# Kernel tuning notes

Hardware: AMD Instinct MI355X
Metric: run time of the kernel (lower is better)

Reference implementation:

```python
import jax, jax.numpy as jnp
import numpy as np

B, N, D, R, NUM_HEADS, S = 8, 512, 256, 6, 3, 1000


def setup_inputs() -> dict:
    key = jax.random.key(0)
    ks = jax.random.split(key, 12)
    init = lambda k, shape: jax.random.normal(k, shape, jnp.float32) * 0.02
    return {
        "symbol_ids": jax.random.randint(ks[0], (B, N), 0, S),
        "positions": jax.random.normal(ks[1], (B, N, 2), jnp.float32),
        "sym_table": init(ks[2], (S, D)),
        "layer_table": init(ks[3], (S, D)),      # layer-0 interpretation embedding
        "rel_W": init(ks[4], (R, D, D)),          # per-relation Linear weights (in,out)
        "rel_b": init(ks[5], (R, D)),
        "h1_W": init(ks[6], (NUM_HEADS, D, D)),   # interpretation head Linear1
        "h1_b": init(ks[7], (NUM_HEADS, D)),
        "h2_W": init(ks[8], (NUM_HEADS, D)),      # interpretation head Linear2 (D->1)
        "h2_b": init(ks[9], (NUM_HEADS,)),
        "out_W": init(ks[10], (D, D)),
        "out_b": init(ks[11], (D,)),
    }


def _relation_type(dx, dy):
    # Vectorized version of PositionalGrammar._get_relation_type (if/elif chain)
    return jnp.select(
        [dy > 0.5, dy < -0.5, dx < -0.5, dx > 0.5,
         (jnp.abs(dx) < 0.3) & (jnp.abs(dy) < 0.3)],
        [0, 1, 2, 3, 4], 5)


def _positional_grammar(symbols, positions, rel_W, rel_b):
    # transformed[b,j] = symbols[b,j] + sum_{i!=j} (symbols[b,i] @ W_r(i,j) + b_r(i,j))
    dx = positions[:, None, :, 0] - positions[:, :, None, 0]  # [b,i,j]
    dy = positions[:, None, :, 1] - positions[:, :, None, 1]
    rel = _relation_type(dx, dy)                               # [b,i,j] int
    n = symbols.shape[1]
    not_self = ~jnp.eye(n, dtype=bool)
    # one-hot relation mask, self-pairs excluded: [b,i,j,r]
    M = ((rel[..., None] == jnp.arange(R)) & not_self[None, :, :, None]).astype(symbols.dtype)
    T = jnp.einsum('bid,rde->brie', symbols, rel_W)            # per-relation transform of sources
    contrib = jnp.einsum('bijr,brie->bje', M, T)               # scatter-add over sources i
    bias = jnp.einsum('bijr,re->bje', M, rel_b)                # per-pair bias accumulation
    return symbols + contrib + bias


def reference(symbol_ids, positions, sym_table, layer_table, rel_W, rel_b,
              h1_W, h1_b, h2_W, h2_b, out_W, out_b):
    # SymbolEmbedding (calendar_pos=None path; layer=0)
    symbols = sym_table[symbol_ids] + layer_table[symbol_ids]  # [B,N,D]
    # PositionalGrammar
    symbols = _positional_grammar(symbols, positions, rel_W, rel_b)
    # LayeredInterpretation: 3 heads of Linear-GELU-Linear(D->1)
    h = jax.nn.gelu(jnp.einsum('bnd,rde->brne', symbols, h1_W)
                    + h1_b[None, :, None, :], approximate=False)
    interp = jnp.einsum('brne,re->brn', h, h2_W) + h2_b[None, :, None]  # [B,3,N]
    # output projection
    output = symbols @ out_W + out_b
    return (output,
            interp[:, 0, :, None],   # exoteric  [B,N,1]
            interp[:, 1, :, None],   # esoteric
            interp[:, 2, :, None],   # sacred
            symbols)
```

## Files before the change

kernel.cpp:

```cpp
#include <hip/hip_runtime.h>
#include <hip/hip_bf16.h>
#include <math.h>

#define BB 8
#define NN 512
#define DD 256
#define BNT 4096

typedef __attribute__((ext_vector_type(8))) short short8;
typedef __attribute__((ext_vector_type(4))) float f32x4;

#define OFF_S0B   0u
#define OFF_TT    524288u
#define OFF_WCT   6815744u
#define OFF_WBT   7012352u
#define OFF_BB    7143424u
#define OFF_REL   7144448u

#define OUT0_OFF   0u
#define INTERP_OFF 1048576u
#define SYM_OFF    1060864u

__device__ __forceinline__ float gelu_exact(float x) {
    return 0.5f * x * (1.0f + erff(x * 0.70710678118654752f));
}

__device__ __forceinline__ ushort f2bf(float x) {
    __hip_bfloat16 h = __float2bfloat16(x);
    union { __hip_bfloat16 b; ushort u; } cv;
    cv.b = h;
    return cv.u;
}

typedef __attribute__((address_space(3))) unsigned int  lds_u32;
typedef __attribute__((address_space(1))) unsigned int  glb_u32;
__device__ __forceinline__ void gload16(const void* g, void* l) {
    __builtin_amdgcn_global_load_lds((const glb_u32*)g, (lds_u32*)l, 16, 0, 0);
}

__device__ __forceinline__ int rel_of(float dx, float dy) {
    int r = (fabsf(dx) < 0.3f && fabsf(dy) < 0.3f) ? 4 : 5;
    r = (dx >  0.5f) ? 3 : r;
    r = (dx < -0.5f) ? 2 : r;
    r = (dy < -0.5f) ? 1 : r;
    r = (dy >  0.5f) ? 0 : r;
    return r;
}

__device__ __forceinline__ short8 onehot8(uint2 cw, unsigned rr) {
    union { ushort u[8]; short8 v; } o;
    unsigned m = rr * 0x01010101u;
    unsigned x = cw.x ^ m, y = cw.y ^ m;
#pragma unroll
    for (int t = 0; t < 4; t++) {
        o.u[t]     = (((x >> (8 * t)) & 255u) == 0u) ? 0x3F80 : 0;
        o.u[t + 4] = (((y >> (8 * t)) & 255u) == 0u) ? 0x3F80 : 0;
    }
    return o.v;
}

#define WAVE_IDS()                                             \
    const int lane = tid & 63, w = tid >> 6;                   \
    const int wm = w >> 1, wn = w & 1;                         \
    const int quad = lane >> 4, l15 = lane & 15;               \
    const int sm = tid >> 2, sq = tid & 3;                     \
    (void)sm; (void)sq;

#define ACC_INIT()                                             \
    f32x4 acc[2][2];                                           \
    _Pragma("unroll") for (int mt = 0; mt < 2; mt++)           \
    _Pragma("unroll") for (int nt = 0; nt < 2; nt++)           \
        acc[mt][nt] = (f32x4){0.f, 0.f, 0.f, 0.f};

#define MFMA4(a0, a1, b0, b1)                                                     \
    acc[0][0] = __builtin_amdgcn_mfma_f32_16x16x32_bf16(a0, b0, acc[0][0], 0, 0, 0); \
    acc[0][1] = __builtin_amdgcn_mfma_f32_16x16x32_bf16(a0, b1, acc[0][1], 0, 0, 0); \
    acc[1][0] = __builtin_amdgcn_mfma_f32_16x16x32_bf16(a1, b0, acc[1][0], 0, 0, 0); \
    acc[1][1] = __builtin_amdgcn_mfma_f32_16x16x32_bf16(a1, b1, acc[1][1], 0, 0, 0);

#define MFMA_STEP(Abuf, Bbuf)                                                \
    {                                                                        \
        short8 af[2], bfr[2];                                                \
        _Pragma("unroll")                                                    \
        for (int mt = 0; mt < 2; mt++)                                       \
            af[mt] = *(const short8*)&(Abuf)[(quad * 64 + wm * 32 + mt * 16 + l15) * 8]; \
        _Pragma("unroll")                                                    \
        for (int nt = 0; nt < 2; nt++)                                       \
            bfr[nt] = *(const short8*)&(Bbuf)[(quad * 64 + wn * 32 + nt * 16 + l15) * 8]; \
        MFMA4(af[0], af[1], bfr[0], bfr[1]);                                 \
    }

__global__ __launch_bounds__(256) void front_kernel(
    const int* __restrict__ ids, const float* __restrict__ positions,
    const float* __restrict__ symt, const float* __restrict__ layt,
    const float* __restrict__ relW, const float* __restrict__ h1W,
    const float* __restrict__ outW, const float* __restrict__ h1b,
    const float* __restrict__ outb, const float* __restrict__ h2b,
    ushort* __restrict__ WcT, ushort* __restrict__ WbT,
    float* __restrict__ bbig, float* __restrict__ outI,
    float* __restrict__ symOut, ushort* __restrict__ s0b,
    unsigned char* __restrict__ rel)
{
    __shared__ float px[NN], py[NN];
    int blk = blockIdx.x, tid = threadIdx.x;
    if (blk < 1536) {
        int idx = blk * 256 + tid;
        {
            int e = idx / 1536, k = idx - e * 1536;
            int r = k >> 8, d = k & 255;
            WcT[idx] = f2bf(relW[(r * DD + d) * DD + e]);
        }
        if (idx < 262144) {
            int c = idx >> 8, d = idx & 255;
            float v;
            if (c < 768) { int r = c >> 8, e = c & 255; v = h1W[(r * DD + d) * DD + e]; }
            else         { v = outW[d * DD + (c - 768)]; }
            WbT[idx] = f2bf(v);
        }
        if (idx < 3 * BNT) outI[idx] = h2b[idx >> 12];
        if (idx < 1024) bbig[idx] = (idx < 768) ? h1b[idx] : outb[idx - 768];
    } else if (blk < 2560) {
        int row = (blk - 1536) * 4 + (tid >> 6);
        int d = (tid & 63) * 4;
        int id = ids[row];
        float4 a = *(const float4*)&symt[(size_t)id * DD + d];
        float4 c = *(const float4*)&layt[(size_t)id * DD + d];
        float4 v = {a.x + c.x, a.y + c.y, a.z + c.z, a.w + c.w};
        *(float4*)&symOut[(size_t)row * DD + d] = v;
        union { ushort u[4]; uint2 q; } p;
        p.u[0] = f2bf(v.x); p.u[1] = f2bf(v.y); p.u[2] = f2bf(v.z); p.u[3] = f2bf(v.w);
        *(uint2*)&s0b[(size_t)row * DD + d] = p.q;
    } else {
        int blk2 = blk - 2560;
        int b = blk2 >> 6;
        int j0 = (blk2 & 63) << 3;
        int jl = tid >> 5, sub = tid & 31;
        for (int i = tid; i < NN; i += 256) {
            float2 p = ((const float2*)positions)[b * NN + i];
            px[i] = p.x; py[i] = p.y;
        }
        __syncthreads();
        int j = j0 + jl;
        float xj = px[j], yj = py[j];
        union { unsigned char u8[16]; uint4 v; } codes;
#pragma unroll
        for (int t = 0; t < 16; t++) {
            int i = sub * 16 + t;
            int r = rel_of(xj - px[i], yj - py[i]);
            r = (i == j) ? 6 : r;
            codes.u8[t] = (unsigned char)r;
        }
        *(uint4*)&rel[((size_t)(b * NN + j)) * NN + sub * 16] = codes.v;
    }
}

__global__ __launch_bounds__(256) void gemmT_kernel(
    const ushort* __restrict__ WcT, const ushort* __restrict__ s0b,
    const float* __restrict__ relb, ushort* __restrict__ TT)
{
    __shared__ ushort Als[2][2048], Bls[2][2048];
    int tid = threadIdx.x;
    int b = blockIdx.z;
    int rowM0 = blockIdx.y * 64;
    int col0 = blockIdx.x * 64;
    int r = rowM0 >> 8, e0 = rowM0 & 255;
    WAVE_IDS();
    ACC_INIT();
    const ushort* gA = WcT + (size_t)(e0 + lane) * 1536 + r * 256 + w * 8;
    const ushort* gB = s0b + ((size_t)(b * NN) + col0 + lane) * DD + w * 8;

    gload16(gA, &Als[0][w * 512]);
    gload16(gB, &Bls[0][w * 512]);
    __syncthreads();
#pragma unroll
    for (int s = 0; s < 8; s++) {
        if (s < 7) {
            gload16(gA + (s + 1) * 32, &Als[(s + 1) & 1][w * 512]);
            gload16(gB + (s + 1) * 32, &Bls[(s + 1) & 1][w * 512]);
        }
        MFMA_STEP(Als[s & 1], Bls[s & 1]);
        __syncthreads();
    }
#pragma unroll
    for (int mt = 0; mt < 2; mt++)
#pragma unroll
        for (int nt = 0; nt < 2; nt++)
#pragma unroll
            for (int v = 0; v < 4; v++) {
                int e = e0 + wm * 32 + mt * 16 + quad * 4 + v;
                int i = col0 + wn * 32 + nt * 16 + l15;
                TT[((size_t)(b * DD) + e) * 3072 + r * 512 + i] =
                    f2bf(acc[mt][nt][v] + relb[r * DD + e]);
            }
}

__global__ __launch_bounds__(256) void agg_gemm(
    const unsigned char* __restrict__ rel, const ushort* __restrict__ TT,
    float* __restrict__ symOut)
{
    __shared__ ushort Bls[2][2048];
    int tid = threadIdx.x;
    int z = blockIdx.z;
    int b = z / 6;
    unsigned rr = (unsigned)(z - b * 6);
    int row0 = blockIdx.y * 64, col0 = blockIdx.x * 64;
    WAVE_IDS();
    ACC_INIT();
    const ushort* gB = TT + ((size_t)(b * DD) + col0 + lane) * 3072 + rr * 512 + w * 8;
    const unsigned char* gC0 = rel + ((size_t)(b * NN) + row0 + wm * 32 + l15) * NN + quad * 8;
    const unsigned char* gC1 = gC0 + 16 * NN;

    gload16(gB, &Bls[0][w * 512]);
    uint2 c0 = *(const uint2*)gC0;
    uint2 c1 = *(const uint2*)gC1;
    __syncthreads();
#pragma unroll
    for (int s = 0; s < 16; s++) {
        uint2 n0 = c0, n1 = c1;
        if (s < 15) {
            gload16(gB + (s + 1) * 32, &Bls[(s + 1) & 1][w * 512]);
            n0 = *(const uint2*)(gC0 + (s + 1) * 32);
            n1 = *(const uint2*)(gC1 + (s + 1) * 32);
        }
        short8 a0 = onehot8(c0, rr);
        short8 a1 = onehot8(c1, rr);
        short8 b0 = *(const short8*)&Bls[s & 1][(quad * 64 + wn * 32 + l15) * 8];
        short8 b1 = *(const short8*)&Bls[s & 1][(quad * 64 + wn * 32 + 16 + l15) * 8];
        MFMA4(a0, a1, b0, b1);
        c0 = n0; c1 = n1;
        __syncthreads();
    }
#pragma unroll
    for (int mt = 0; mt < 2; mt++)
#pragma unroll
        for (int nt = 0; nt < 2; nt++)
#pragma unroll
            for (int v = 0; v < 4; v++) {
                int j = row0 + wm * 32 + mt * 16 + quad * 4 + v;
                int e = col0 + wn * 32 + nt * 16 + l15;
                atomicAdd(&symOut[((size_t)(b * NN) + j) * DD + e], acc[mt][nt][v]);
            }
}

__global__ __launch_bounds__(256) void gemm2_kernel(
    const float* __restrict__ symOut, const ushort* __restrict__ WbT,
    const float* __restrict__ bbig, const float* __restrict__ h2W,
    float* __restrict__ out0, float* __restrict__ outI)
{
    __shared__ ushort Als[2][2048], Bls[2][2048];
    int tid = threadIdx.x;
    int row0 = blockIdx.y * 64, col0 = blockIdx.x * 64;
    WAVE_IDS();
    ACC_INIT();
    const float*  gA = symOut + (size_t)(row0 + sm) * DD + sq * 8;
    const ushort* gB = WbT + (size_t)(col0 + lane) * DD + w * 8;
    const int lo = (sq * 64 + sm) * 8;

#define G2_STAGE(a0, a1, buf)                                       \
    {                                                               \
        union alignas(16) { ushort u[8]; uint4 v; } am;             \
        am.u[0] = f2bf(a0.x); am.u[1] = f2bf(a0.y);                 \
        am.u[2] = f2bf(a0.z); am.u[3] = f2bf(a0.w);                 \
        am.u[4] = f2bf(a1.x); am.u[5] = f2bf(a1.y);                 \
        am.u[6] = f2bf(a1.z); am.u[7] = f2bf(a1.w);                 \
        *(uint4*)&Als[buf][lo] = am.v;                              \
    }

    float4 a0 = *(const float4*)gA;
    float4 a1 = *(const float4*)(gA + 4);
    gload16(gB, &Bls[0][w * 512]);
    G2_STAGE(a0, a1, 0);
    __syncthreads();
#pragma unroll
    for (int s = 0; s < 8; s++) {
        float4 x = a0, y = a1;
        if (s < 7) {
            x = *(const float4*)(gA + (s + 1) * 32);
            y = *(const float4*)(gA + (s + 1) * 32 + 4);
            gload16(gB + (s + 1) * 32, &Bls[(s + 1) & 1][w * 512]);
        }
        MFMA_STEP(Als[s & 1], Bls[s & 1]);
        if (s < 7) { G2_STAGE(x, y, (s + 1) & 1); }
        __syncthreads();
    }
#undef G2_STAGE
    if (col0 >= 768) {
#pragma unroll
        for (int nt = 0; nt < 2; nt++) {
            int c = col0 + wn * 32 + nt * 16 + l15;
            float bb = bbig[c];
#pragma unroll
            for (int mt = 0; mt < 2; mt++)
#pragma unroll
                for (int v = 0; v < 4; v++) {
                    int row = row0 + wm * 32 + mt * 16 + quad * 4 + v;
                    out0[(size_t)row * DD + (c - 768)] = acc[mt][nt][v] + bb;
                }
        }
    } else {
        int head = col0 >> 8;
        float part[2][4];
#pragma unroll
        for (int mt = 0; mt < 2; mt++)
#pragma unroll
            for (int v = 0; v < 4; v++) part[mt][v] = 0.f;
#pragma unroll
        for (int nt = 0; nt < 2; nt++) {
            int c = col0 + wn * 32 + nt * 16 + l15;
            float bb = bbig[c];
            float w2 = h2W[c];
#pragma unroll
            for (int mt = 0; mt < 2; mt++)
#pragma unroll
                for (int v = 0; v < 4; v++)
                    part[mt][v] += gelu_exact(acc[mt][nt][v] + bb) * w2;
        }
#pragma unroll
        for (int mt = 0; mt < 2; mt++)
#pragma unroll
            for (int v = 0; v < 4; v++) {
                float p = part[mt][v];
                p += __shfl_xor(p, 1); p += __shfl_xor(p, 2);
                p += __shfl_xor(p, 4); p += __shfl_xor(p, 8);
                if (l15 == 0) {
                    int row = row0 + wm * 32 + mt * 16 + quad * 4 + v;
                    atomicAdd(&outI[head * BNT + row], p);
                }
            }
    }
}

extern "C" void kernel_launch(void* const* d_in, const int* in_sizes, int n_in,
                              void* d_out, int out_size, void* d_ws, size_t ws_size,
                              hipStream_t stream)
{
    const int*   ids  = (const int*)d_in[0];
    const float* pos  = (const float*)d_in[1];
    const float* symt = (const float*)d_in[2];
    const float* layt = (const float*)d_in[3];
    const float* relW = (const float*)d_in[4];
    const float* relb = (const float*)d_in[5];
    const float* h1W  = (const float*)d_in[6];
    const float* h1b  = (const float*)d_in[7];
    const float* h2W  = (const float*)d_in[8];
    const float* h2b  = (const float*)d_in[9];
    const float* outW = (const float*)d_in[10];
    const float* outb = (const float*)d_in[11];
    float* out = (float*)d_out;
    float* ws  = (float*)d_ws;

    ushort* s0b  = (ushort*)(ws + OFF_S0B);
    ushort* TT   = (ushort*)(ws + OFF_TT);
    ushort* WcT  = (ushort*)(ws + OFF_WCT);
    ushort* WbT  = (ushort*)(ws + OFF_WBT);
    float*  bbig = ws + OFF_BB;
    unsigned char* rel = (unsigned char*)(ws + OFF_REL);

    front_kernel<<<3072, 256, 0, stream>>>(ids, pos, symt, layt, relW, h1W, outW,
                                           h1b, outb, h2b, WcT, WbT, bbig,
                                           out + INTERP_OFF, out + SYM_OFF, s0b, rel);
    gemmT_kernel<<<dim3(8, 24, 8), 256, 0, stream>>>(WcT, s0b, relb, TT);
    agg_gemm<<<dim3(4, 8, 48), 256, 0, stream>>>(rel, TT, out + SYM_OFF);
    gemm2_kernel<<<dim3(16, 64), 256, 0, stream>>>(out + SYM_OFF, WbT,
                                                   bbig, h2W,
                                                   out + OUT0_OFF, out + INTERP_OFF);
}
```

Measured before the change: 157.7 us.

## Reorder relation aggregation before projection and compute bias from relation counts

The relation step now aggregates raw symbols per relation first (one-hot mask times transposed bf16 symbols) and then applies a single concatenated 4096x1536x256 projection against the stacked relation weights. This replaces the per-relation transform of all sources (the large TT buffer) followed by atomic scatter-adds. Per-target relation counts are computed with byte-match popcounts in the front kernel and turn the bias sum into six multiply-adds. The projection kernel does plain read-modify-write instead of atomics. The trade-off is an extra bf16 rounding of the aggregated Gc intermediate and a K=1536 GEMM with larger shared-memory tiles.

Result: slower. 163.0 us (+3.3%).

```diff
diff --git a/kernel.cpp b/kernel.cpp
--- a/kernel.cpp
+++ b/kernel.cpp
@@ -10,12 +10,13 @@
 typedef __attribute__((ext_vector_type(8))) short short8;
 typedef __attribute__((ext_vector_type(4))) float f32x4;
 
-#define OFF_S0B   0u
-#define OFF_TT    524288u
-#define OFF_WCT   6815744u
-#define OFF_WBT   7012352u
-#define OFF_BB    7143424u
-#define OFF_REL   7144448u
+#define OFF_S0T   0u
+#define OFF_GC    524288u
+#define OFF_WCT   3670016u
+#define OFF_WBT   3866624u
+#define OFF_BB    3997696u
+#define OFF_CNT   3998720u
+#define OFF_REL   4015104u
 
 #define OUT0_OFF   0u
 #define INTERP_OFF 1048576u
@@ -57,6 +58,10 @@
         o.u[t + 4] = (((y >> (8 * t)) & 255u) == 0u) ? 0x3F80 : 0;
     }
     return o.v;
+}
+
+__device__ __forceinline__ unsigned zbyte_mask(unsigned t) {
+    return ~(((t & 0x7F7F7F7Fu) + 0x7F7F7F7Fu) | t) & 0x80808080u;
 }
 
 #define WAVE_IDS()                                             \
@@ -98,10 +103,10 @@
     const float* __restrict__ outb, const float* __restrict__ h2b,
     ushort* __restrict__ WcT, ushort* __restrict__ WbT,
     float* __restrict__ bbig, float* __restrict__ outI,
-    float* __restrict__ symOut, ushort* __restrict__ s0b,
-    unsigned char* __restrict__ rel)
+    float* __restrict__ symOut, ushort* __restrict__ s0T,
+    unsigned char* __restrict__ rel, ushort* __restrict__ cnts)
 {
-    __shared__ float px[NN], py[NN];
+    __shared__ float shbuf[32 * 257];
     int blk = blockIdx.x, tid = threadIdx.x;
     if (blk < 1536) {
         int idx = blk * 256 + tid;
@@ -119,19 +124,36 @@
         }
         if (idx < 3 * BNT) outI[idx] = h2b[idx >> 12];
         if (idx < 1024) bbig[idx] = (idx < 768) ? h1b[idx] : outb[idx - 768];
-    } else if (blk < 2560) {
-        int row = (blk - 1536) * 4 + (tid >> 6);
-        int d = (tid & 63) * 4;
+    } else if (blk < 1664) {
+        int row0 = (blk - 1536) * 32;
+        int b = row0 >> 9, i0 = row0 & 511;
+        int rl = tid >> 3, dq = (tid & 7) * 4;
+        int row = row0 + rl;
         int id = ids[row];
-        float4 a = *(const float4*)&symt[(size_t)id * DD + d];
-        float4 c = *(const float4*)&layt[(size_t)id * DD + d];
-        float4 v = {a.x + c.x, a.y + c.y, a.z + c.z, a.w + c.w};
-        *(float4*)&symOut[(size_t)row * DD + d] = v;
-        union { ushort u[4]; uint2 q; } p;
-        p.u[0] = f2bf(v.x); p.u[1] = f2bf(v.y); p.u[2] = f2bf(v.z); p.u[3] = f2bf(v.w);
-        *(uint2*)&s0b[(size_t)row * DD + d] = p.q;
+#pragma unroll
+        for (int u = 0; u < 8; u++) {
+            int d = dq + u * 32;
+            float4 a = *(const float4*)&symt[(size_t)id * DD + d];
+            float4 c = *(const float4*)&layt[(size_t)id * DD + d];
+            float4 v = {a.x + c.x, a.y + c.y, a.z + c.z, a.w + c.w};
+            *(float4*)&symOut[(size_t)row * DD + d] = v;
+            shbuf[rl * 257 + d + 0] = v.x;
+            shbuf[rl * 257 + d + 1] = v.y;
+            shbuf[rl * 257 + d + 2] = v.z;
+            shbuf[rl * 257 + d + 3] = v.w;
+        }
+        __syncthreads();
+        int dd = tid;
+        union { ushort u[32]; uint4 q[4]; } pk;
+#pragma unroll
+        for (int ii = 0; ii < 32; ii++) pk.u[ii] = f2bf(shbuf[ii * 257 + dd]);
+        ushort* dst = s0T + ((size_t)(b * DD + dd)) * 512 + i0;
+#pragma unroll
+        for (int q = 0; q < 4; q++) ((uint4*)dst)[q] = pk.q[q];
     } else {
-        int blk2 = blk - 2560;
+        float* px = shbuf;
+        float* py = shbuf + NN;
+        int blk2 = blk - 1664;
         int b = blk2 >> 6;
         int j0 = (blk2 & 63) << 3;
         int jl = tid >> 5, sub = tid & 31;
@@ -142,7 +164,7 @@
         __syncthreads();
         int j = j0 + jl;
         float xj = px[j], yj = py[j];
-        union { unsigned char u8[16]; uint4 v; } codes;
+        union { unsigned char u8[16]; unsigned wd[4]; uint4 v; } codes;
 #pragma unroll
         for (int t = 0; t < 16; t++) {
             int i = sub * 16 + t;
@@ -151,85 +173,87 @@
             codes.u8[t] = (unsigned char)r;
         }
         *(uint4*)&rel[((size_t)(b * NN + j)) * NN + sub * 16] = codes.v;
-    }
-}
-
-__global__ __launch_bounds__(256) void gemmT_kernel(
-    const ushort* __restrict__ WcT, const ushort* __restrict__ s0b,
-    const float* __restrict__ relb, ushort* __restrict__ TT)
+        int cnt[6];
+#pragma unroll
+        for (int r = 0; r < 6; r++) {
+            unsigned m = (unsigned)r * 0x01010101u;
+            int c = 0;
+#pragma unroll
+            for (int k = 0; k < 4; k++)
+                c += __builtin_popcount(zbyte_mask(codes.wd[k] ^ m));
+            cnt[r] = c;
+        }
+#pragma unroll
+        for (int r = 0; r < 6; r++) {
+            cnt[r] += __shfl_xor(cnt[r], 1);
+            cnt[r] += __shfl_xor(cnt[r], 2);
+            cnt[r] += __shfl_xor(cnt[r], 4);
+            cnt[r] += __shfl_xor(cnt[r], 8);
+            cnt[r] += __shfl_xor(cnt[r], 16);
+        }
+        if (sub == 0) {
+            uint4 pq;
+            pq.x = (unsigned)cnt[0] | ((unsigned)cnt[1] << 16);
+            pq.y = (unsigned)cnt[2] | ((unsigned)cnt[3] << 16);
+            pq.z = (unsigned)cnt[4] | ((unsigned)cnt[5] << 16);
+            pq.w = 0u;
+            *(uint4*)&cnts[((size_t)(b * NN + j)) * 8] = pq;
+        }
+    }
+}
+
+__global__ __launch_bounds__(256) void aggT_kernel(
+    const unsigned char* __restrict__ rel, const ushort* __restrict__ s0T,
+    ushort* __restrict__ Gc)
 {
-    __shared__ ushort Als[2][2048], Bls[2][2048];
-    int tid = threadIdx.x;
-    int b = blockIdx.z;
-    int rowM0 = blockIdx.y * 64;
-    int col0 = blockIdx.x * 64;
-    int r = rowM0 >> 8, e0 = rowM0 & 255;
-    WAVE_IDS();
-    ACC_INIT();
-    const ushort* gA = WcT + (size_t)(e0 + lane) * 1536 + r * 256 + w * 8;
-    const ushort* gB = s0b + ((size_t)(b * NN) + col0 + lane) * DD + w * 8;
-
-    gload16(gA, &Als[0][w * 512]);
-    gload16(gB, &Bls[0][w * 512]);
-    __syncthreads();
-#pragma unroll
-    for (int s = 0; s < 8; s++) {
-        if (s < 7) {
-            gload16(gA + (s + 1) * 32, &Als[(s + 1) & 1][w * 512]);
-            gload16(gB + (s + 1) * 32, &Bls[(s + 1) & 1][w * 512]);
-        }
-        MFMA_STEP(Als[s & 1], Bls[s & 1]);
-        __syncthreads();
-    }
-#pragma unroll
-    for (int mt = 0; mt < 2; mt++)
-#pragma unroll
-        for (int nt = 0; nt < 2; nt++)
-#pragma unroll
-            for (int v = 0; v < 4; v++) {
-                int e = e0 + wm * 32 + mt * 16 + quad * 4 + v;
-                int i = col0 + wn * 32 + nt * 16 + l15;
-                TT[((size_t)(b * DD) + e) * 3072 + r * 512 + i] =
-                    f2bf(acc[mt][nt][v] + relb[r * DD + e]);
-            }
-}
-
-__global__ __launch_bounds__(256) void agg_gemm(
-    const unsigned char* __restrict__ rel, const ushort* __restrict__ TT,
-    float* __restrict__ symOut)
-{
-    __shared__ ushort Bls[2][2048];
+    __shared__ ushort Bls[2][4096];
     int tid = threadIdx.x;
     int z = blockIdx.z;
     int b = z / 6;
     unsigned rr = (unsigned)(z - b * 6);
-    int row0 = blockIdx.y * 64, col0 = blockIdx.x * 64;
+    int row0 = blockIdx.y * 64;
+    int col0 = blockIdx.x * 64;
     WAVE_IDS();
     ACC_INIT();
-    const ushort* gB = TT + ((size_t)(b * DD) + col0 + lane) * 3072 + rr * 512 + w * 8;
+    const ushort* gB = s0T + ((size_t)(b * DD) + col0 + lane) * 512 + w * 8;
     const unsigned char* gC0 = rel + ((size_t)(b * NN) + row0 + wm * 32 + l15) * NN + quad * 8;
     const unsigned char* gC1 = gC0 + 16 * NN;
 
-    gload16(gB, &Bls[0][w * 512]);
-    uint2 c0 = *(const uint2*)gC0;
-    uint2 c1 = *(const uint2*)gC1;
+#define AGT_STAGE(s, buf)                                     \
+    gload16(gB + (s) * 64,      &Bls[buf][ w      * 512]);    \
+    gload16(gB + (s) * 64 + 32, &Bls[buf][(w + 4) * 512]);
+
+    uint2 cc[2][2], cn[2][2];
+    cc[0][0] = *(const uint2*)(gC0);
+    cc[0][1] = *(const uint2*)(gC0 + 32);
+    cc[1][0] = *(const uint2*)(gC1);
+    cc[1][1] = *(const uint2*)(gC1 + 32);
+    AGT_STAGE(0, 0);
     __syncthreads();
 #pragma unroll
-    for (int s = 0; s < 16; s++) {
-        uint2 n0 = c0, n1 = c1;
-        if (s < 15) {
-            gload16(gB + (s + 1) * 32, &Bls[(s + 1) & 1][w * 512]);
-            n0 = *(const uint2*)(gC0 + (s + 1) * 32);
-            n1 = *(const uint2*)(gC1 + (s + 1) * 32);
-        }
-        short8 a0 = onehot8(c0, rr);
-        short8 a1 = onehot8(c1, rr);
-        short8 b0 = *(const short8*)&Bls[s & 1][(quad * 64 + wn * 32 + l15) * 8];
-        short8 b1 = *(const short8*)&Bls[s & 1][(quad * 64 + wn * 32 + 16 + l15) * 8];
-        MFMA4(a0, a1, b0, b1);
-        c0 = n0; c1 = n1;
+    for (int s = 0; s < 8; s++) {
+        if (s < 7) {
+            AGT_STAGE(s + 1, (s + 1) & 1);
+            cn[0][0] = *(const uint2*)(gC0 + (s + 1) * 64);
+            cn[0][1] = *(const uint2*)(gC0 + (s + 1) * 64 + 32);
+            cn[1][0] = *(const uint2*)(gC1 + (s + 1) * 64);
+            cn[1][1] = *(const uint2*)(gC1 + (s + 1) * 64 + 32);
+        }
+#pragma unroll
+        for (int h = 0; h < 2; h++) {
+            short8 a0 = onehot8(cc[0][h], rr);
+            short8 a1 = onehot8(cc[1][h], rr);
+            short8 b0 = *(const short8*)&Bls[s & 1][((h * 4 + quad) * 64 + wn * 32 + l15) * 8];
+            short8 b1 = *(const short8*)&Bls[s & 1][((h * 4 + quad) * 64 + wn * 32 + 16 + l15) * 8];
+            MFMA4(a0, a1, b0, b1);
+        }
+        if (s < 7) {
+            cc[0][0] = cn[0][0]; cc[0][1] = cn[0][1];
+            cc[1][0] = cn[1][0]; cc[1][1] = cn[1][1];
+        }
         __syncthreads();
     }
+#undef AGT_STAGE
 #pragma unroll
     for (int mt = 0; mt < 2; mt++)
 #pragma unroll
@@ -237,9 +261,67 @@
 #pragma unroll
             for (int v = 0; v < 4; v++) {
                 int j = row0 + wm * 32 + mt * 16 + quad * 4 + v;
+                int d = col0 + wn * 32 + nt * 16 + l15;
+                Gc[((size_t)(b * NN) + j) * 1536 + rr * 256 + d] =
+                    f2bf(acc[mt][nt][v]);
+            }
+}
+
+__global__ __launch_bounds__(256) void projC_kernel(
+    const ushort* __restrict__ Gc, const ushort* __restrict__ WcT,
+    const ushort* __restrict__ cnts, const float* __restrict__ relb,
+    float* __restrict__ symOut)
+{
+    __shared__ ushort Als[2][8192], Bls[2][8192];
+    int tid = threadIdx.x;
+    int row0 = blockIdx.y * 64;
+    int col0 = blockIdx.x * 64;
+    WAVE_IDS();
+    ACC_INIT();
+    const ushort* gA = Gc  + (size_t)(row0 + lane) * 1536 + w * 8;
+    const ushort* gB = WcT + (size_t)(col0 + lane) * 1536 + w * 8;
+
+#define PJ_STAGE(s, buf)                                                    \
+    _Pragma("unroll")                                                       \
+    for (int p = 0; p < 4; p++) {                                           \
+        gload16(gA + (s) * 128 + p * 32, &Als[buf][(w + p * 4) * 512]);     \
+        gload16(gB + (s) * 128 + p * 32, &Bls[buf][(w + p * 4) * 512]);     \
+    }
+
+    PJ_STAGE(0, 0);
+    __syncthreads();
+#pragma unroll
+    for (int s = 0; s < 12; s++) {
+        if (s < 11) { PJ_STAGE(s + 1, (s + 1) & 1); }
+#pragma unroll
+        for (int h = 0; h < 4; h++) {
+            short8 a0 = *(const short8*)&Als[s & 1][((h * 4 + quad) * 64 + wm * 32 + l15) * 8];
+            short8 a1 = *(const short8*)&Als[s & 1][((h * 4 + quad) * 64 + wm * 32 + 16 + l15) * 8];
+            short8 b0 = *(const short8*)&Bls[s & 1][((h * 4 + quad) * 64 + wn * 32 + l15) * 8];
+            short8 b1 = *(const short8*)&Bls[s & 1][((h * 4 + quad) * 64 + wn * 32 + 16 + l15) * 8];
+            MFMA4(a0, a1, b0, b1);
+        }
+        __syncthreads();
+    }
+#undef PJ_STAGE
+#pragma unroll
+    for (int mt = 0; mt < 2; mt++)
+#pragma unroll
+        for (int v = 0; v < 4; v++) {
+            int row = row0 + wm * 32 + mt * 16 + quad * 4 + v;
+            const ushort* cp = &cnts[(size_t)row * 8];
+            float c0 = cp[0], c1 = cp[1], c2 = cp[2];
+            float c3 = cp[3], c4 = cp[4], c5 = cp[5];
+#pragma unroll
+            for (int nt = 0; nt < 2; nt++) {
                 int e = col0 + wn * 32 + nt * 16 + l15;
-                atomicAdd(&symOut[((size_t)(b * NN) + j) * DD + e], acc[mt][nt][v]);
+                float bias = c0 * relb[e]            + c1 * relb[DD + e]
+                           + c2 * relb[2 * DD + e]   + c3 * relb[3 * DD + e]
+                           + c4 * relb[4 * DD + e]   + c5 * relb[5 * DD + e];
+                float* po = &symOut[(size_t)row * DD + e];
+                *po = *po + acc[mt][nt][v] + bias;
             }
+        }
 }
 
 __global__ __launch_bounds__(256) void gemm2_kernel(
@@ -349,18 +431,21 @@
     float* out = (float*)d_out;
     float* ws  = (float*)d_ws;
 
-    ushort* s0b  = (ushort*)(ws + OFF_S0B);
-    ushort* TT   = (ushort*)(ws + OFF_TT);
+    ushort* s0T  = (ushort*)(ws + OFF_S0T);
+    ushort* Gc   = (ushort*)(ws + OFF_GC);
     ushort* WcT  = (ushort*)(ws + OFF_WCT);
     ushort* WbT  = (ushort*)(ws + OFF_WBT);
     float*  bbig = ws + OFF_BB;
+    ushort* cnts = (ushort*)(ws + OFF_CNT);
     unsigned char* rel = (unsigned char*)(ws + OFF_REL);
 
-    front_kernel<<<3072, 256, 0, stream>>>(ids, pos, symt, layt, relW, h1W, outW,
+    front_kernel<<<2176, 256, 0, stream>>>(ids, pos, symt, layt, relW, h1W, outW,
                                            h1b, outb, h2b, WcT, WbT, bbig,
-                                           out + INTERP_OFF, out + SYM_OFF, s0b, rel);
-    gemmT_kernel<<<dim3(8, 24, 8), 256, 0, stream>>>(WcT, s0b, relb, TT);
-    agg_gemm<<<dim3(4, 8, 48), 256, 0, stream>>>(rel, TT, out + SYM_OFF);
+                                           out + INTERP_OFF, out + SYM_OFF, s0T,
+                                           rel, cnts);
+    aggT_kernel<<<dim3(4, 8, 48), 256, 0, stream>>>(rel, s0T, Gc);
+    projC_kernel<<<dim3(4, 64), 256, 0, stream>>>(Gc, WcT, cnts, relb,
+                                                  out + SYM_OFF);
     gemm2_kernel<<<dim3(16, 64), 256, 0, stream>>>(out + SYM_OFF, WbT,
                                                    bbig, h2W,
                                                    out + OUT0_OFF, out + INTERP_OFF);
```
